# Kernel tuning notes

Measured on AMD Instinct MI355X. Metric: run time of the kernel, lower is better.

## Reference

```python
import jax, jax.numpy as jnp
import numpy as np


def _conv3d(x, w, b, pad_t):
    # x: (b, c, t, h, w); w: (out_c, in_c, kt, 1, 1); conv only along time dim
    y = jax.lax.conv_general_dilated(
        x, w, window_strides=(1, 1, 1),
        padding=((pad_t, pad_t), (0, 0), (0, 0)),
        dimension_numbers=('NCDHW', 'OIDHW', 'NCDHW'))
    return y + b[None, :, None, None, None]


def setup_inputs() -> dict:
    key = jax.random.key(0)
    ks = jax.random.split(key, 8)
    b, t, c, h, w = 4, 16, 64, 96, 96
    cq = c // 8
    s = 0.05
    return {
        'x': jax.random.normal(ks[0], (b, t, c, h, w), jnp.float32),
        'wq': jax.random.normal(ks[1], (cq, c, 3, 1, 1), jnp.float32) * s,
        'bq': jax.random.normal(ks[2], (cq,), jnp.float32) * s,
        'wk': jax.random.normal(ks[3], (cq, c, 3, 1, 1), jnp.float32) * s,
        'bk': jax.random.normal(ks[4], (cq,), jnp.float32) * s,
        'wv': jax.random.normal(ks[5], (c, c, 1, 1, 1), jnp.float32) * s,
        'bv': jax.random.normal(ks[6], (c,), jnp.float32) * s,
        'gamma': jax.random.normal(ks[7], (1,), jnp.float32) * 0.1,
    }


def reference(x, wq, bq, wk, bk, wv, bv, gamma):
    b, t, c, h, w = x.shape
    xc = jnp.transpose(x, (0, 2, 1, 3, 4))  # (b, c, t, h, w)
    # q, k: (b, t, c//8 * h * w); v: (b, t, c * h * w)
    q = jnp.transpose(_conv3d(xc, wq, bq, 1), (0, 2, 1, 3, 4)).reshape(b, t, -1)
    k = jnp.transpose(_conv3d(xc, wk, bk, 1), (0, 2, 1, 3, 4)).reshape(b, t, -1)
    v = jnp.transpose(_conv3d(xc, wv, bv, 0), (0, 2, 1, 3, 4)).reshape(b, t, -1)
    energy = jnp.einsum('btd,bsd->bts', q, k)          # (b, t, t)
    heat = jax.nn.softmax(energy, axis=-1)             # softmax over dim 2
    out = jnp.einsum('bts,bsd->btd', heat, v).reshape(b, t, c, h, w)
    return gamma * out + x
```

## Files before the change

### kernel.cpp

```cpp
#include <hip/hip_runtime.h>
#include <math.h>

#define B_  4
#define T_  16
#define C_  64
#define CQ_ 8
#define HW_ 9216
#define NCHUNK_ 288

typedef __attribute__((ext_vector_type(8))) short    s16x8;
typedef __attribute__((ext_vector_type(4))) float    f32x4;
typedef __attribute__((ext_vector_type(4))) unsigned u32x4;

static __device__ __forceinline__ short f2bf(float f) {
  union { float f; unsigned u; } v; v.f = f;
  return (short)((v.u + 0x7FFFu + ((v.u >> 16) & 1u)) >> 16);
}
static __device__ __forceinline__ unsigned pkbf(float lo, float hi) {
  unsigned r;
  asm("v_cvt_pk_bf16_f32 %0, %1, %2" : "=v"(r) : "v"(lo), "v"(hi));
  return r;
}

__global__ __launch_bounds__(256)
void k_prep(const float* __restrict__ wq, const float* __restrict__ wk,
            const float* __restrict__ wv, float* __restrict__ WT,
            short* __restrict__ wvb) {
  for (int j = threadIdx.x; j < CQ_ * C_ * 3; j += 256) {
    int ci = j / 24, r = j % 24;
    int cqi = r / 3, d = r % 3;
    WT[ci * 32 + r]        = wq[(cqi * C_ + ci) * 3 + d];
    WT[2048 + ci * 32 + r] = wk[(cqi * C_ + ci) * 3 + d];
  }
  for (int idx = threadIdx.x; idx < 4096; idx += 256) {
    int j = idx & 7, lane = (idx >> 3) & 63, fr = idx >> 9;
    int ct = fr >> 1, ks = fr & 1;
    int c  = ct * 16 + (lane & 15);
    int ci = ks * 32 + (lane >> 4) * 8 + j;
    wvb[idx] = f2bf(wv[c * C_ + ci]);
  }
}

__global__ __launch_bounds__(512, 4)
void k_energy(const float* __restrict__ x, const float* __restrict__ WT,
              const float* __restrict__ bq, const float* __restrict__ bk,
              float* __restrict__ partE) {
  __shared__ __attribute__((aligned(16))) float QK[2 * 32 * 196];
  __shared__ float Etmp[256];

  const int b   = blockIdx.y;
  const int hw0 = blockIdx.x * 32;
  const int tid = threadIdx.x;
  const int t = tid >> 5;
  const int g = tid & 31;
  const float* xb  = x + (size_t)(b * T_ * C_) * HW_ + hw0 + g;
  const float* wqt = WT;
  const float* wkt = WT + 2048;

  float qa[CQ_], ka[CQ_];
#pragma unroll
  for (int j = 0; j < CQ_; ++j) { qa[j] = 0.f; ka[j] = 0.f; }

#pragma unroll 2
  for (int ci = 0; ci < C_; ++ci) {
    float xm = 0.f, xp = 0.f;
    if (t > 0)      xm = xb[(size_t)((t - 1) * C_ + ci) * HW_];
    float x0 =           xb[(size_t)(t * C_ + ci) * HW_];
    if (t < T_ - 1) xp = xb[(size_t)((t + 1) * C_ + ci) * HW_];
    const float* wq_r = &wqt[ci * 32];
    const float* wk_r = &wkt[ci * 32];
#pragma unroll
    for (int j = 0; j < CQ_; ++j) {
      qa[j] += wq_r[j * 3 + 0] * xm + wq_r[j * 3 + 1] * x0 + wq_r[j * 3 + 2] * xp;
      ka[j] += wk_r[j * 3 + 0] * xm + wk_r[j * 3 + 1] * x0 + wk_r[j * 3 + 2] * xp;
    }
  }
#pragma unroll
  for (int j = 0; j < CQ_; ++j) { qa[j] += bq[j]; ka[j] += bk[j]; }

  float* Qs = &QK[0];
  float* Ks = &QK[32 * 196];
#pragma unroll
  for (int j = 0; j < CQ_; ++j) {
    Qs[g * 196 + t * 12 + j] = qa[j];
    Ks[g * 196 + t * 12 + j] = ka[j];
  }
  __syncthreads();

  const int h  = tid >> 8;
  const int tt = (tid >> 4) & 15;
  const int ss = tid & 15;
  float e = 0.f;
  for (int gg = h * 16; gg < h * 16 + 16; ++gg) {
    const float4 q0 = *(const float4*)&Qs[gg * 196 + tt * 12];
    const float4 q1 = *(const float4*)&Qs[gg * 196 + tt * 12 + 4];
    const float4 k0 = *(const float4*)&Ks[gg * 196 + ss * 12];
    const float4 k1 = *(const float4*)&Ks[gg * 196 + ss * 12 + 4];
    e += q0.x * k0.x + q0.y * k0.y + q0.z * k0.z + q0.w * k0.w
       + q1.x * k1.x + q1.y * k1.y + q1.z * k1.z + q1.w * k1.w;
  }
  if (h == 1) Etmp[tt * 16 + ss] = e;
  __syncthreads();
  if (h == 0) {
    e += Etmp[tt * 16 + ss];
    partE[((size_t)(b * NCHUNK_ + blockIdx.x)) * 256 + tt * 16 + ss] = e;
  }
}

__global__ __launch_bounds__(256)
void k_softmax(const float* __restrict__ partE, float* __restrict__ heat) {
  const int b = blockIdx.x;
  const int tid = threadIdx.x;
  float e = 0.f;
  for (int ch = 0; ch < NCHUNK_; ++ch)
    e += partE[((size_t)(b * NCHUNK_ + ch)) * 256 + tid];
  float mx = e;
#pragma unroll
  for (int m = 1; m < 16; m <<= 1) mx = fmaxf(mx, __shfl_xor(mx, m, 64));
  float ex = expf(e - mx);
  float sm = ex;
#pragma unroll
  for (int m = 1; m < 16; m <<= 1) sm += __shfl_xor(sm, m, 64);
  heat[b * 256 + tid] = ex / sm;
}

__global__ __launch_bounds__(256, 3)
void k_mix(const float* __restrict__ x, const float* __restrict__ heat,
           const short* __restrict__ wvb, const float* __restrict__ bv,
           const float* __restrict__ gam, float* __restrict__ out) {
  __shared__ __attribute__((aligned(16))) short sm[20480];

  const int b    = blockIdx.y;
  const int hw0  = blockIdx.x * 16;
  const int tid  = threadIdx.x;
  const int lane = tid & 63;
  const int w    = tid >> 6;
  const int l15  = lane & 15;
  const int lq   = lane >> 4;

  union U8 { s16x8 v; int i[4]; unsigned u[4]; };
  const f32x4 fz = {0.f, 0.f, 0.f, 0.f};

  U8 ha; ha.i[0] = ha.i[1] = ha.i[2] = ha.i[3] = 0;
  if (lane < 32) {
    const float* hp = heat + b * 256 + l15 * 16 + lq * 8;
    float4 h0 = *(const float4*)hp;
    float4 h1 = *(const float4*)(hp + 4);
    ha.u[0] = pkbf(h0.x, h0.y); ha.u[1] = pkbf(h0.z, h0.w);
    ha.u[2] = pkbf(h1.x, h1.y); ha.u[3] = pkbf(h1.z, h1.w);
  }

  {
    const int ci = tid >> 2, q = tid & 3;
    const int sx = ci & 7;
    const float* xp = x + ((size_t)b * T_ * C_ + ci) * HW_ + hw0 + q * 4;
    short* r0 = &sm[(ci * 16 + q * 4) * 20];
#pragma unroll
    for (int P = 0; P < 8; ++P) {
      float4 v0 = *(const float4*)(xp + (size_t)(2 * P) * C_ * HW_);
      float4 v1 = *(const float4*)(xp + (size_t)(2 * P + 1) * C_ * HW_);
      const int ip = (P ^ sx) * 2;
      *(unsigned*)&r0[ip]      = pkbf(v0.x, v1.x);
      *(unsigned*)&r0[20 + ip] = pkbf(v0.y, v1.y);
      *(unsigned*)&r0[40 + ip] = pkbf(v0.z, v1.z);
      *(unsigned*)&r0[60 + ip] = pkbf(v0.w, v1.w);
    }
  }

  U8 a2[8];
#pragma unroll
  for (int fr = 0; fr < 8; ++fr)
    a2[fr].v = *(const s16x8*)&wvb[(fr * 64 + lane) * 8];

  asm volatile("s_waitcnt lgkmcnt(0)" ::: "memory");

  const int lq2 = lq & 1;
  f32x4 c1[16];
#pragma unroll
  for (int i = 0; i < 16; ++i) {
    const int ci = w * 16 + i;
    const short* row = &sm[(ci * 16 + l15) * 20];
    const int base = (lq2 * 4) ^ (i & 4);
    int2 D0 = *(const int2*)&row[2 * base];
    int2 D1 = *(const int2*)&row[2 * base + 4];
    U8 bx;
    const int t3 = i & 3;
    bx.i[0] = (t3 == 0) ? D0.x : (t3 == 1) ? D0.y : (t3 == 2) ? D1.x : D1.y;
    bx.i[1] = (t3 == 0) ? D0.y : (t3 == 1) ? D0.x : (t3 == 2) ? D1.y : D1.x;
    bx.i[2] = (t3 == 0) ? D1.x : (t3 == 1) ? D1.y : (t3 == 2) ? D0.x : D0.y;
    bx.i[3] = (t3 == 0) ? D1.y : (t3 == 1) ? D1.x : (t3 == 2) ? D0.y : D0.x;
    c1[i] = __builtin_amdgcn_mfma_f32_16x16x32_bf16(ha.v, bx.v, fz, 0, 0, 0);
  }
  __syncthreads();

  unsigned rc[32];
#pragma unroll
  for (int ct = 0; ct < 4; ++ct)
#pragma unroll
    for (int r = 0; r < 4; ++r) {
      const int c = ct * 16 + lq * 4 + r;
      const short* row = &sm[(c * 16 + l15) * 20];
      const int base = 4 * ((w >> 1) ^ (lq & 1)) + 2 * ((w & 1) ^ (r >> 1));
      int2 D = *(const int2*)&row[2 * base];
      rc[(ct * 4 + r) * 2 + 0] = (r & 1) ? (unsigned)D.y : (unsigned)D.x;
      rc[(ct * 4 + r) * 2 + 1] = (r & 1) ? (unsigned)D.x : (unsigned)D.y;
    }
  __syncthreads();

#pragma unroll
  for (int r = 0; r < 4; ++r) {
    const int t = lq * 4 + r;
    short* dst = &sm[(t * 16 + l15) * 72 + w * 16];
    u32x4 p0, p1;
    p0[0] = pkbf(c1[0][r],  c1[1][r]);  p0[1] = pkbf(c1[2][r],  c1[3][r]);
    p0[2] = pkbf(c1[4][r],  c1[5][r]);  p0[3] = pkbf(c1[6][r],  c1[7][r]);
    p1[0] = pkbf(c1[8][r],  c1[9][r]);  p1[1] = pkbf(c1[10][r], c1[11][r]);
    p1[2] = pkbf(c1[12][r], c1[13][r]); p1[3] = pkbf(c1[14][r], c1[15][r]);
    *(u32x4*)dst       = p0;
    *(u32x4*)(dst + 8) = p1;
  }

  f32x4 bvr[4];
#pragma unroll
  for (int ct = 0; ct < 4; ++ct)
    bvr[ct] = *(const f32x4*)(bv + ct * 16 + lq * 4);
  const float gamma = gam[0];
  __syncthreads();

#pragma unroll
  for (int ntq = 0; ntq < 4; ++ntq) {
    const int t = w * 4 + ntq;
    const short* xr0 = &sm[(t * 16 + l15) * 72];
    s16x8 b0 = *(const s16x8*)(xr0 + lq * 8);
    s16x8 b1 = *(const s16x8*)(xr0 + 32 + lq * 8);
    float* op = out + ((size_t)(b * T_ + t) * C_) * HW_ + hw0 + l15;
    const int half = ntq >> 1, odd = ntq & 1;
#pragma unroll
    for (int ct = 0; ct < 4; ++ct) {
      f32x4 acc = __builtin_amdgcn_mfma_f32_16x16x32_bf16(a2[ct * 2 + 0].v, b0, fz, 0, 0, 0);
      acc = __builtin_amdgcn_mfma_f32_16x16x32_bf16(a2[ct * 2 + 1].v, b1, acc, 0, 0, 0);
      const int cb = ct * 16 + lq * 4;
#pragma unroll
      for (int r = 0; r < 4; ++r) {
        const unsigned v = rc[(ct * 4 + r) * 2 + half];
        union { unsigned u; float f; } z;
        z.u = odd ? (v & 0xffff0000u) : (v << 16);
        op[(size_t)(cb + r) * HW_] = gamma * (acc[r] + bvr[ct][r]) + z.f;
      }
    }
  }
}

extern "C" void kernel_launch(void* const* d_in, const int* in_sizes, int n_in,
                              void* d_out, int out_size, void* d_ws, size_t ws_size,
                              hipStream_t stream) {
  const float* x   = (const float*)d_in[0];
  const float* wq  = (const float*)d_in[1];
  const float* bq  = (const float*)d_in[2];
  const float* wk  = (const float*)d_in[3];
  const float* bk  = (const float*)d_in[4];
  const float* wv  = (const float*)d_in[5];
  const float* bv  = (const float*)d_in[6];
  const float* gam = (const float*)d_in[7];
  float* out = (float*)d_out;

  float* WT    = (float*)d_ws;
  short* wvb   = (short*)(WT + 4096);
  float* partE = WT + 4096 + 2048;
  float* heat  = partE + (size_t)B_ * NCHUNK_ * 256;

  k_prep   <<<1, 256, 0, stream>>>(wq, wk, wv, WT, wvb);
  k_energy <<<dim3(NCHUNK_, B_), 512, 0, stream>>>(x, WT, bq, bk, partE);
  k_softmax<<<dim3(B_),          256, 0, stream>>>(partE, heat);
  k_mix    <<<dim3(HW_ / 16, B_), 256, 0, stream>>>(x, heat, wvb, bv, gam, out);
}
```

Measured before the change: 175.5 us.

## Compute energy partials with split-bf16 MFMA and two pixels per thread

Each energy block now covers 64 pixels, with each thread loading float2 pairs so it computes Q/K for two adjacent pixels. This halves the number of blocks and the partial-energy buffer the softmax kernel has to reduce. The per-chunk Q·K^T reduction moves from scalar LDS float4 dot products to bf16 MFMA. Q and K are stored as hi/lo bf16 pairs in swizzled shared memory, and three MFMAs are used to keep accuracy close to fp32. The risks are a small precision loss from the dropped lo·lo term and lower parallelism from having half as many blocks.

```diff
diff --git a/kernel.cpp b/kernel.cpp
--- a/kernel.cpp
+++ b/kernel.cpp
@@ -6,7 +6,7 @@
 #define C_  64
 #define CQ_ 8
 #define HW_ 9216
-#define NCHUNK_ 288
+#define NCH2_ 144
 
 typedef __attribute__((ext_vector_type(8))) short    s16x8;
 typedef __attribute__((ext_vector_type(4))) float    f32x4;
@@ -20,6 +20,9 @@
   unsigned r;
   asm("v_cvt_pk_bf16_f32 %0, %1, %2" : "=v"(r) : "v"(lo), "v"(hi));
   return r;
+}
+static __device__ __forceinline__ float ubf(unsigned u) {
+  union { unsigned u; float f; } v; v.u = u; return v.f;
 }
 
 __global__ __launch_bounds__(256)
@@ -45,65 +48,88 @@
 void k_energy(const float* __restrict__ x, const float* __restrict__ WT,
               const float* __restrict__ bq, const float* __restrict__ bk,
               float* __restrict__ partE) {
-  __shared__ __attribute__((aligned(16))) float QK[2 * 32 * 196];
-  __shared__ float Etmp[256];
+  __shared__ __attribute__((aligned(16))) short QKs[32768];
+  __shared__ float Ered[8 * 256];
 
   const int b   = blockIdx.y;
-  const int hw0 = blockIdx.x * 32;
+  const int hw0 = blockIdx.x * 64;
   const int tid = threadIdx.x;
-  const int t = tid >> 5;
-  const int g = tid & 31;
-  const float* xb  = x + (size_t)(b * T_ * C_) * HW_ + hw0 + g;
+  const int t   = tid >> 5;
+  const int gq  = tid & 31;
+
+  const float* xb  = x + (size_t)(b * T_ * C_) * HW_ + hw0 + 2 * gq;
   const float* wqt = WT;
   const float* wkt = WT + 2048;
 
-  float qa[CQ_], ka[CQ_];
-#pragma unroll
-  for (int j = 0; j < CQ_; ++j) { qa[j] = 0.f; ka[j] = 0.f; }
+  float2 qa[CQ_], ka[CQ_];
+#pragma unroll
+  for (int j = 0; j < CQ_; ++j) {
+    qa[j].x = qa[j].y = 0.f; ka[j].x = ka[j].y = 0.f;
+  }
 
 #pragma unroll 2
   for (int ci = 0; ci < C_; ++ci) {
-    float xm = 0.f, xp = 0.f;
-    if (t > 0)      xm = xb[(size_t)((t - 1) * C_ + ci) * HW_];
-    float x0 =           xb[(size_t)(t * C_ + ci) * HW_];
-    if (t < T_ - 1) xp = xb[(size_t)((t + 1) * C_ + ci) * HW_];
+    float2 xm = {0.f, 0.f}, xp = {0.f, 0.f};
+    if (t > 0)      xm = *(const float2*)(xb + (size_t)((t - 1) * C_ + ci) * HW_);
+    float2 x0 =          *(const float2*)(xb + (size_t)(t * C_ + ci) * HW_);
+    if (t < T_ - 1) xp = *(const float2*)(xb + (size_t)((t + 1) * C_ + ci) * HW_);
     const float* wq_r = &wqt[ci * 32];
     const float* wk_r = &wkt[ci * 32];
 #pragma unroll
     for (int j = 0; j < CQ_; ++j) {
-      qa[j] += wq_r[j * 3 + 0] * xm + wq_r[j * 3 + 1] * x0 + wq_r[j * 3 + 2] * xp;
-      ka[j] += wk_r[j * 3 + 0] * xm + wk_r[j * 3 + 1] * x0 + wk_r[j * 3 + 2] * xp;
+      const float a0 = wq_r[j * 3 + 0], a1 = wq_r[j * 3 + 1], a2 = wq_r[j * 3 + 2];
+      qa[j].x += a0 * xm.x + a1 * x0.x + a2 * xp.x;
+      qa[j].y += a0 * xm.y + a1 * x0.y + a2 * xp.y;
+      const float c0 = wk_r[j * 3 + 0], c1 = wk_r[j * 3 + 1], c2 = wk_r[j * 3 + 2];
+      ka[j].x += c0 * xm.x + c1 * x0.x + c2 * xp.x;
+      ka[j].y += c0 * xm.y + c1 * x0.y + c2 * xp.y;
     }
   }
-#pragma unroll
-  for (int j = 0; j < CQ_; ++j) { qa[j] += bq[j]; ka[j] += bk[j]; }
-
-  float* Qs = &QK[0];
-  float* Ks = &QK[32 * 196];
+
+  const int gof = ((gq >> 2) ^ (t & 7)) * 8 + 2 * (gq & 3);
 #pragma unroll
   for (int j = 0; j < CQ_; ++j) {
-    Qs[g * 196 + t * 12 + j] = qa[j];
-    Ks[g * 196 + t * 12 + j] = ka[j];
-  }
-  __syncthreads();
-
-  const int h  = tid >> 8;
-  const int tt = (tid >> 4) & 15;
-  const int ss = tid & 15;
-  float e = 0.f;
-  for (int gg = h * 16; gg < h * 16 + 16; ++gg) {
-    const float4 q0 = *(const float4*)&Qs[gg * 196 + tt * 12];
-    const float4 q1 = *(const float4*)&Qs[gg * 196 + tt * 12 + 4];
-    const float4 k0 = *(const float4*)&Ks[gg * 196 + ss * 12];
-    const float4 k1 = *(const float4*)&Ks[gg * 196 + ss * 12 + 4];
-    e += q0.x * k0.x + q0.y * k0.y + q0.z * k0.z + q0.w * k0.w
-       + q1.x * k1.x + q1.y * k1.y + q1.z * k1.z + q1.w * k1.w;
-  }
-  if (h == 1) Etmp[tt * 16 + ss] = e;
-  __syncthreads();
-  if (h == 0) {
-    e += Etmp[tt * 16 + ss];
-    partE[((size_t)(b * NCHUNK_ + blockIdx.x)) * 256 + tt * 16 + ss] = e;
+    const float q0 = qa[j].x + bq[j], q1 = qa[j].y + bq[j];
+    const float k0 = ka[j].x + bk[j], k1 = ka[j].y + bk[j];
+    const unsigned qh = pkbf(q0, q1);
+    const unsigned ql = pkbf(q0 - ubf(qh << 16), q1 - ubf(qh & 0xffff0000u));
+    const unsigned kh = pkbf(k0, k1);
+    const unsigned kl = pkbf(k0 - ubf(kh << 16), k1 - ubf(kh & 0xffff0000u));
+    const int rb = (t * 8 + j) * 64 + gof;
+    *(unsigned*)&QKs[rb]         = qh;
+    *(unsigned*)&QKs[8192 + rb]  = ql;
+    *(unsigned*)&QKs[16384 + rb] = kh;
+    *(unsigned*)&QKs[24576 + rb] = kl;
+  }
+  __syncthreads();
+
+  const int lane = tid & 63, w = tid >> 6;
+  const int l15  = lane & 15, lq = lane >> 4;
+  f32x4 acc = {0.f, 0.f, 0.f, 0.f};
+#pragma unroll
+  for (int kk = 0; kk < 2; ++kk) {
+    const int ks = w * 2 + kk;
+    const int cq = ks >> 1;
+    const int g0 = (ks & 1) * 32 + lq * 8;
+    const int rb = (l15 * 8 + cq) * 64 + (((g0 >> 3) ^ (l15 & 7)) << 3);
+    s16x8 fqh = *(const s16x8*)&QKs[rb];
+    s16x8 fql = *(const s16x8*)&QKs[8192 + rb];
+    s16x8 fkh = *(const s16x8*)&QKs[16384 + rb];
+    s16x8 fkl = *(const s16x8*)&QKs[24576 + rb];
+    acc = __builtin_amdgcn_mfma_f32_16x16x32_bf16(fqh, fkh, acc, 0, 0, 0);
+    acc = __builtin_amdgcn_mfma_f32_16x16x32_bf16(fqh, fkl, acc, 0, 0, 0);
+    acc = __builtin_amdgcn_mfma_f32_16x16x32_bf16(fql, fkh, acc, 0, 0, 0);
+  }
+#pragma unroll
+  for (int r = 0; r < 4; ++r)
+    Ered[w * 256 + (lq * 4 + r) * 16 + l15] = acc[r];
+  __syncthreads();
+
+  if (tid < 256) {
+    float e = 0.f;
+#pragma unroll
+    for (int ww = 0; ww < 8; ++ww) e += Ered[ww * 256 + tid];
+    partE[((size_t)(b * NCH2_ + blockIdx.x)) * 256 + tid] = e;
   }
 }
 
@@ -112,8 +138,8 @@
   const int b = blockIdx.x;
   const int tid = threadIdx.x;
   float e = 0.f;
-  for (int ch = 0; ch < NCHUNK_; ++ch)
-    e += partE[((size_t)(b * NCHUNK_ + ch)) * 256 + tid];
+  for (int ch = 0; ch < NCH2_; ++ch)
+    e += partE[((size_t)(b * NCH2_ + ch)) * 256 + tid];
   float mx = e;
 #pragma unroll
   for (int m = 1; m < 16; m <<= 1) mx = fmaxf(mx, __shfl_xor(mx, m, 64));
@@ -267,10 +293,10 @@
   float* WT    = (float*)d_ws;
   short* wvb   = (short*)(WT + 4096);
   float* partE = WT + 4096 + 2048;
-  float* heat  = partE + (size_t)B_ * NCHUNK_ * 256;
+  float* heat  = partE + (size_t)B_ * NCH2_ * 256;
 
   k_prep   <<<1, 256, 0, stream>>>(wq, wk, wv, WT, wvb);
-  k_energy <<<dim3(NCHUNK_, B_), 512, 0, stream>>>(x, WT, bq, bk, partE);
-  k_softmax<<<dim3(B_),          256, 0, stream>>>(partE, heat);
+  k_energy <<<dim3(NCH2_, B_), 512, 0, stream>>>(x, WT, bq, bk, partE);
+  k_softmax<<<dim3(B_),        256, 0, stream>>>(partE, heat);
   k_mix    <<<dim3(HW_ / 16, B_), 256, 0, stream>>>(x, heat, wvb, bv, gam, out);
 }
```

Result: faster. 169.2 us (-3.6%).

## Compute Q/K temporal conv and energy with bf16 MFMA in k_energy

Applied to the files above, without the earlier changes.

Rewrites the energy kernel so the 3-tap temporal conv producing Q and K runs as bf16 MFMA over an LDS-staged, XOR-swizzled x tile. The Q·K^T energy is also done with MFMA, using a hi/lo bf16 split to recover precision. Tiles shrink to 16 pixels, doubling the chunk count and the partial-energy reduction in softmax. This replaces the scalar fp32 FMA conv loop with matrix-core work, at the cost of bf16 rounding in Q/K and a larger partial buffer.

```diff
diff --git a/kernel.cpp b/kernel.cpp
--- a/kernel.cpp
+++ b/kernel.cpp
@@ -6,7 +6,7 @@
 #define C_  64
 #define CQ_ 8
 #define HW_ 9216
-#define NCHUNK_ 288
+#define NCH_ 576
 
 typedef __attribute__((ext_vector_type(8))) short    s16x8;
 typedef __attribute__((ext_vector_type(4))) float    f32x4;
@@ -21,16 +21,22 @@
   asm("v_cvt_pk_bf16_f32 %0, %1, %2" : "=v"(r) : "v"(lo), "v"(hi));
   return r;
 }
+static __device__ __forceinline__ float ubf(unsigned u) {
+  union { unsigned u; float f; } v; v.u = u; return v.f;
+}
 
 __global__ __launch_bounds__(256)
 void k_prep(const float* __restrict__ wq, const float* __restrict__ wk,
-            const float* __restrict__ wv, float* __restrict__ WT,
+            const float* __restrict__ wv, short* __restrict__ wqkb,
             short* __restrict__ wvb) {
-  for (int j = threadIdx.x; j < CQ_ * C_ * 3; j += 256) {
-    int ci = j / 24, r = j % 24;
-    int cqi = r / 3, d = r % 3;
-    WT[ci * 32 + r]        = wq[(cqi * C_ + ci) * 3 + d];
-    WT[2048 + ci * 32 + r] = wk[(cqi * C_ + ci) * 3 + d];
+  for (int idx = threadIdx.x; idx < 3072; idx += 256) {
+    int j = idx & 7, lane = (idx >> 3) & 63, ks = idx >> 9;
+    int m = lane & 15, lq = lane >> 4;
+    int ci = (ks & 1) * 32 + lq * 8 + j;
+    int d  = ks >> 1;
+    float wval = (m < 8) ? wq[(m * C_ + ci) * 3 + d]
+                         : wk[((m - 8) * C_ + ci) * 3 + d];
+    wqkb[idx] = f2bf(wval);
   }
   for (int idx = threadIdx.x; idx < 4096; idx += 256) {
     int j = idx & 7, lane = (idx >> 3) & 63, fr = idx >> 9;
@@ -42,68 +48,98 @@
 }
 
 __global__ __launch_bounds__(512, 4)
-void k_energy(const float* __restrict__ x, const float* __restrict__ WT,
+void k_energy(const float* __restrict__ x, const short* __restrict__ wqkb,
               const float* __restrict__ bq, const float* __restrict__ bk,
               float* __restrict__ partE) {
-  __shared__ __attribute__((aligned(16))) float QK[2 * 32 * 196];
-  __shared__ float Etmp[256];
-
-  const int b   = blockIdx.y;
-  const int hw0 = blockIdx.x * 32;
-  const int tid = threadIdx.x;
-  const int t = tid >> 5;
-  const int g = tid & 31;
-  const float* xb  = x + (size_t)(b * T_ * C_) * HW_ + hw0 + g;
-  const float* wqt = WT;
-  const float* wkt = WT + 2048;
-
-  float qa[CQ_], ka[CQ_];
-#pragma unroll
-  for (int j = 0; j < CQ_; ++j) { qa[j] = 0.f; ka[j] = 0.f; }
-
-#pragma unroll 2
-  for (int ci = 0; ci < C_; ++ci) {
-    float xm = 0.f, xp = 0.f;
-    if (t > 0)      xm = xb[(size_t)((t - 1) * C_ + ci) * HW_];
-    float x0 =           xb[(size_t)(t * C_ + ci) * HW_];
-    if (t < T_ - 1) xp = xb[(size_t)((t + 1) * C_ + ci) * HW_];
-    const float* wq_r = &wqt[ci * 32];
-    const float* wk_r = &wkt[ci * 32];
-#pragma unroll
-    for (int j = 0; j < CQ_; ++j) {
-      qa[j] += wq_r[j * 3 + 0] * xm + wq_r[j * 3 + 1] * x0 + wq_r[j * 3 + 2] * xp;
-      ka[j] += wk_r[j * 3 + 0] * xm + wk_r[j * 3 + 1] * x0 + wk_r[j * 3 + 2] * xp;
-    }
-  }
-#pragma unroll
-  for (int j = 0; j < CQ_; ++j) { qa[j] += bq[j]; ka[j] += bk[j]; }
-
-  float* Qs = &QK[0];
-  float* Ks = &QK[32 * 196];
-#pragma unroll
-  for (int j = 0; j < CQ_; ++j) {
-    Qs[g * 196 + t * 12 + j] = qa[j];
-    Ks[g * 196 + t * 12 + j] = ka[j];
-  }
-  __syncthreads();
-
-  const int h  = tid >> 8;
-  const int tt = (tid >> 4) & 15;
-  const int ss = tid & 15;
-  float e = 0.f;
-  for (int gg = h * 16; gg < h * 16 + 16; ++gg) {
-    const float4 q0 = *(const float4*)&Qs[gg * 196 + tt * 12];
-    const float4 q1 = *(const float4*)&Qs[gg * 196 + tt * 12 + 4];
-    const float4 k0 = *(const float4*)&Ks[gg * 196 + ss * 12];
-    const float4 k1 = *(const float4*)&Ks[gg * 196 + ss * 12 + 4];
-    e += q0.x * k0.x + q0.y * k0.y + q0.z * k0.z + q0.w * k0.w
-       + q1.x * k1.x + q1.y * k1.y + q1.z * k1.z + q1.w * k1.w;
-  }
-  if (h == 1) Etmp[tt * 16 + ss] = e;
-  __syncthreads();
-  if (h == 0) {
-    e += Etmp[tt * 16 + ss];
-    partE[((size_t)(b * NCHUNK_ + blockIdx.x)) * 256 + tt * 16 + ss] = e;
+  __shared__ __attribute__((aligned(16))) short sh[29440];
+  __shared__ float Ered[1024];
+
+  const int b    = blockIdx.y;
+  const int hw0  = blockIdx.x * 16;
+  const int tid  = threadIdx.x;
+  const int lane = tid & 63, w = tid >> 6;
+  const int l15  = lane & 15, lq = lane >> 4;
+  const f32x4 fz = {0.f, 0.f, 0.f, 0.f};
+
+  for (int i = tid; i < 1152; i += 512)
+    ((unsigned*)sh)[(i < 576) ? i : (9216 + i)] = 0;
+
+  s16x8 afr[6];
+#pragma unroll
+  for (int ks = 0; ks < 6; ++ks)
+    afr[ks] = *(const s16x8*)&wqkb[(ks * 64 + lane) * 8];
+
+  const float* bias = (lq < 2) ? bq : bk;
+  const int cqb = (lq & 1) * 4;
+  const float b0 = bias[cqb + 0], b1 = bias[cqb + 1];
+  const float b2 = bias[cqb + 2], b3 = bias[cqb + 3];
+
+  {
+    const int q4 = tid & 3;
+    const int cp = (tid >> 2) & 31;
+    const int s0 = tid >> 7;
+    const float* xb = x + (size_t)(b * T_ * C_ + 2 * cp) * HW_ + hw0 + 4 * q4;
+#pragma unroll
+    for (int it = 0; it < 4; ++it) {
+      const int s = s0 * 4 + it;
+      float4 v0 = *(const float4*)(xb + (size_t)(s * C_) * HW_);
+      float4 v1 = *(const float4*)(xb + (size_t)(s * C_) * HW_ + HW_);
+      const int off = ((cp >> 2) ^ ((s + 1) & 7)) * 8 + 2 * (cp & 3);
+      const int rb  = (s + 1) * 16 + 4 * q4;
+      *(unsigned*)&sh[(rb + 0) * 72 + off] = pkbf(v0.x, v1.x);
+      *(unsigned*)&sh[(rb + 1) * 72 + off] = pkbf(v0.y, v1.y);
+      *(unsigned*)&sh[(rb + 2) * 72 + off] = pkbf(v0.z, v1.z);
+      *(unsigned*)&sh[(rb + 3) * 72 + off] = pkbf(v0.w, v1.w);
+    }
+  }
+  __syncthreads();
+
+#pragma unroll
+  for (int gl = 0; gl < 2; ++gl) {
+    const int g = w * 2 + gl;
+    f32x4 a = fz;
+#pragma unroll
+    for (int ks = 0; ks < 6; ++ks) {
+      const int d = ks >> 1;
+      const int row = (l15 + d) * 16 + g;
+      const int chunk = (((ks & 1) * 4 + lq) ^ ((l15 + d) & 7));
+      s16x8 bf = *(const s16x8*)&sh[row * 72 + chunk * 8];
+      a = __builtin_amdgcn_mfma_f32_16x16x32_bf16(afr[ks], bf, a, 0, 0, 0);
+    }
+    const float v0 = a[0] + b0, v1 = a[1] + b1;
+    const float v2 = a[2] + b2, v3 = a[3] + b3;
+    const unsigned h01 = pkbf(v0, v1), h23 = pkbf(v2, v3);
+    const unsigned l01 = pkbf(v0 - ubf(h01 << 16), v1 - ubf(h01 & 0xffff0000u));
+    const unsigned l23 = pkbf(v2 - ubf(h23 << 16), v3 - ubf(h23 & 0xffff0000u));
+    short* pl = &sh[20736 + (lq >> 1) * 4352 + l15 * 136 + g * 8 + (lq & 1) * 4];
+    uint2 hh; hh.x = h01; hh.y = h23;
+    uint2 ll; ll.x = l01; ll.y = l23;
+    *(uint2*)pl          = hh;
+    *(uint2*)(pl + 2176) = ll;
+  }
+  __syncthreads();
+
+  if (w < 4) {
+    const int off = l15 * 136 + w * 32 + lq * 8;
+    const short* Qp = &sh[20736];
+    const short* Kp = &sh[20736 + 4352];
+    s16x8 qh = *(const s16x8*)&Qp[off];
+    s16x8 ql = *(const s16x8*)&Qp[off + 2176];
+    s16x8 kh = *(const s16x8*)&Kp[off];
+    s16x8 kl = *(const s16x8*)&Kp[off + 2176];
+    f32x4 e = fz;
+    e = __builtin_amdgcn_mfma_f32_16x16x32_bf16(qh, kh, e, 0, 0, 0);
+    e = __builtin_amdgcn_mfma_f32_16x16x32_bf16(qh, kl, e, 0, 0, 0);
+    e = __builtin_amdgcn_mfma_f32_16x16x32_bf16(ql, kh, e, 0, 0, 0);
+#pragma unroll
+    for (int r = 0; r < 4; ++r)
+      Ered[w * 256 + (lq * 4 + r) * 16 + l15] = e[r];
+  }
+  __syncthreads();
+
+  if (tid < 256) {
+    float e = Ered[tid] + Ered[256 + tid] + Ered[512 + tid] + Ered[768 + tid];
+    partE[((size_t)(b * NCH_ + blockIdx.x)) * 256 + tid] = e;
   }
 }
 
@@ -112,8 +148,8 @@
   const int b = blockIdx.x;
   const int tid = threadIdx.x;
   float e = 0.f;
-  for (int ch = 0; ch < NCHUNK_; ++ch)
-    e += partE[((size_t)(b * NCHUNK_ + ch)) * 256 + tid];
+  for (int ch = 0; ch < NCH_; ++ch)
+    e += partE[((size_t)(b * NCH_ + ch)) * 256 + tid];
   float mx = e;
 #pragma unroll
   for (int m = 1; m < 16; m <<= 1) mx = fmaxf(mx, __shfl_xor(mx, m, 64));
@@ -264,13 +300,13 @@
   const float* gam = (const float*)d_in[7];
   float* out = (float*)d_out;
 
-  float* WT    = (float*)d_ws;
-  short* wvb   = (short*)(WT + 4096);
-  float* partE = WT + 4096 + 2048;
-  float* heat  = partE + (size_t)B_ * NCHUNK_ * 256;
-
-  k_prep   <<<1, 256, 0, stream>>>(wq, wk, wv, WT, wvb);
-  k_energy <<<dim3(NCHUNK_, B_), 512, 0, stream>>>(x, WT, bq, bk, partE);
-  k_softmax<<<dim3(B_),          256, 0, stream>>>(partE, heat);
+  short* wqkb  = (short*)d_ws;
+  short* wvb   = wqkb + 3072;
+  float* partE = (float*)(wvb + 4096 + 1024);
+  float* heat  = partE + (size_t)B_ * NCH_ * 256;
+
+  k_prep   <<<1, 256, 0, stream>>>(wq, wk, wv, wqkb, wvb);
+  k_energy <<<dim3(NCH_, B_), 512, 0, stream>>>(x, wqkb, bq, bk, partE);
+  k_softmax<<<dim3(B_),       256, 0, stream>>>(partE, heat);
   k_mix    <<<dim3(HW_ / 16, B_), 256, 0, stream>>>(x, heat, wvb, bv, gam, out);
 }
```

Measured after the change: 153.8 us. 12.4% less time.
